# Kernel optimization log

Measured on AMD Instinct MI355X. Metric: run time of the kernel, lower is better.

The kernel has to match this reference:

```python
import jax, jax.numpy as jnp
import numpy as np

B, N, M, C = 2, 8192, 1024, 1152  # batch, dense points, centers, feature dim
K = 3                              # three_nn interpolation
EPS = 1e-8


def setup_inputs() -> dict:
    key = jax.random.key(0)
    k1, k2, k3 = jax.random.split(key, 3)
    xyz = jax.random.normal(k1, (B, N, 3), dtype=jnp.float32)      # query points
    center = jax.random.normal(k2, (B, M, 3), dtype=jnp.float32)   # center coords (already permuted to B,M,3)
    feats = jax.random.normal(k3, (B, C, M), dtype=jnp.float32)    # backbone features at centers
    return {"xyz": xyz, "center": center, "feats": feats}


def _interpolate(xyz, center, feats):
    # Squared pairwise distances [B, N, M] (PointNet++ three_nn uses squared dists).
    d2 = (jnp.sum(xyz * xyz, axis=-1, keepdims=True)
          + jnp.sum(center * center, axis=-1)[:, None, :]
          - 2.0 * jnp.einsum('bnd,bmd->bnm', xyz, center))
    neg_top, idx = jax.lax.top_k(-d2, K)          # 3 nearest centers per point
    dist = -neg_top                                # [B, N, K] squared distances
    recip = 1.0 / (dist + EPS)
    weight = recip / jnp.sum(recip, axis=-1, keepdims=True)  # [B, N, K]
    fm = jnp.transpose(feats, (0, 2, 1))           # [B, M, C]
    batch_idx = jnp.arange(B)[:, None, None]       # broadcast gather over batch
    gathered = fm[batch_idx, idx]                  # [B, N, K, C]
    out = jnp.einsum('bnkc,bnk->bcn', gathered, weight)  # [B, C, N]
    return out


def reference(xyz, center, feats):
    return _interpolate(xyz, center, feats)
```

## Files before the change

kernel.cpp:

```cpp
#include <hip/hip_runtime.h>
#include <cstdint>

#define B_ 2
#define N_ 8192
#define M_ 1024
#define C_ 1152
#define EPS_ 1e-8f
#define NT 32
#define CHUNK 128
#define NBN (N_ / NT)
#define NBC (C_ / CHUNK)
#define PTS 16
#define TRB ((M_ / 64) * (C_ / 64) * B_)

typedef float f32x4 __attribute__((ext_vector_type(4)));

__device__ __forceinline__ unsigned short f2bf(float f) {
    unsigned u = __float_as_uint(f);
    u += 0x7fffu + ((u >> 16) & 1u);
    return (unsigned short)(u >> 16);
}
__device__ __forceinline__ float bf2f(unsigned short h) {
    return __uint_as_float(((unsigned)h) << 16);
}

__device__ __forceinline__ void ins3(float d, int i,
        float& d0, int& i0, float& d1, int& i1, float& d2, int& i2) {
    bool b0 = d < d0;
    bool b1 = d < d1;
    bool b2 = d < d2;
    d2 = b1 ? d1 : (b2 ? d : d2);   i2 = b1 ? i1 : (b2 ? i : i2);
    d1 = b0 ? d0 : (b1 ? d : d1);   i1 = b0 ? i0 : (b1 ? i : i1);
    d0 = b0 ? d  : d0;              i0 = b0 ? i  : i0;
}
__device__ __forceinline__ void ins3lex(float d, int i,
        float& d0, int& i0, float& d1, int& i1, float& d2, int& i2) {
    bool b0 = (d < d0) || (d == d0 && i < i0);
    bool b1 = (d < d1) || (d == d1 && i < i1);
    bool b2 = (d < d2) || (d == d2 && i < i2);
    d2 = b1 ? d1 : (b2 ? d : d2);   i2 = b1 ? i1 : (b2 ? i : i2);
    d1 = b0 ? d0 : (b1 ? d : d1);   i1 = b0 ? i0 : (b1 ? i : i1);
    d0 = b0 ? d  : d0;              i0 = b0 ? i  : i0;
}

__global__ __launch_bounds__(256) void k_front(const float* __restrict__ feats,
                                               unsigned short* __restrict__ fm,
                                               const float* __restrict__ xyz,
                                               const float* __restrict__ center,
                                               int* __restrict__ idx_ws,
                                               float* __restrict__ w_ws) {
    __shared__ float4 sc[1040];
    int bid = blockIdx.x;
    int t   = threadIdx.x;

    if (bid < TRB) {
        float* tile = (float*)sc;
        int within = bid % ((M_ / 64) * (C_ / 64));
        int b  = bid / ((M_ / 64) * (C_ / 64));
        int mb = within & 15;
        int cb = within >> 4;
        int m0 = mb * 64;
        int c0 = cb * 64;
        int tx = t & 63;
        int ty = t >> 6;
        const float* src = feats + ((size_t)b * C_ + c0) * M_ + m0;
#pragma unroll
        for (int j = 0; j < 16; ++j) {
            int cl = ty + 4 * j;
            tile[cl * 65 + tx] = __builtin_nontemporal_load(&src[(size_t)cl * M_ + tx]);
        }
        __syncthreads();
        unsigned short* dst = fm + ((size_t)b * M_ + m0) * C_ + c0;
#pragma unroll
        for (int j = 0; j < 16; ++j) {
            int ml = ty + 4 * j;
            dst[(size_t)ml * C_ + tx] = f2bf(tile[tx * 65 + ml]);
        }
        return;
    }

    int flat = bid - TRB;
    int b    = flat >> 9;
    int n0   = (flat & 511) * PTS;
    for (int i = t; i < M_; i += 256) {
        float cx = center[((size_t)b * M_ + i) * 3 + 0];
        float cy = center[((size_t)b * M_ + i) * 3 + 1];
        float cz = center[((size_t)b * M_ + i) * 3 + 2];
        float cc = __fadd_rn(__fadd_rn(__fmul_rn(cx, cx), __fmul_rn(cy, cy)),
                             __fmul_rn(cz, cz));
        sc[i] = make_float4(cx, cy, cz, cc);
    }
    __syncthreads();

    int p = t >> 4;
    int c = t & 15;
    int n = n0 + p;
    float x = xyz[((size_t)b * N_ + n) * 3 + 0];
    float y = xyz[((size_t)b * N_ + n) * 3 + 1];
    float z = xyz[((size_t)b * N_ + n) * 3 + 2];
    float xx = __fadd_rn(__fadd_rn(__fmul_rn(x, x), __fmul_rn(y, y)),
                         __fmul_rn(z, z));

    float d0 = __builtin_inff(), d1 = __builtin_inff(), d2 = __builtin_inff();
    int   i0 = 0x7fffffff,  i1 = 0x7fffffff,  i2 = 0x7fffffff;
#pragma unroll 4
    for (int it = 0; it < M_ / 16; ++it) {
        int m = c + it * 16;
        float4 v = sc[m];
        float dot = __fmaf_rn(z, v.z, __fmaf_rn(y, v.y, __fmul_rn(x, v.x)));
        float d   = __fsub_rn(__fadd_rn(xx, v.w), __fmul_rn(2.0f, dot));
        ins3(d, m, d0, i0, d1, i1, d2, i2);
    }
#pragma unroll
    for (int off = 1; off <= 8; off <<= 1) {
        float e0 = __shfl_xor(d0, off); int j0 = __shfl_xor(i0, off);
        float e1 = __shfl_xor(d1, off); int j1 = __shfl_xor(i1, off);
        float e2 = __shfl_xor(d2, off); int j2 = __shfl_xor(i2, off);
        ins3lex(e0, j0, d0, i0, d1, i1, d2, i2);
        ins3lex(e1, j1, d0, i0, d1, i1, d2, i2);
        ins3lex(e2, j2, d0, i0, d1, i1, d2, i2);
    }
    if (c == 0) {
        float r0 = 1.0f / __fadd_rn(d0, EPS_);
        float r1 = 1.0f / __fadd_rn(d1, EPS_);
        float r2 = 1.0f / __fadd_rn(d2, EPS_);
        float s  = __fadd_rn(__fadd_rn(r0, r1), r2);
        size_t base = ((size_t)b * N_ + n) * 3;
        idx_ws[base + 0] = i0; idx_ws[base + 1] = i1; idx_ws[base + 2] = i2;
        w_ws[base + 0] = r0 / s; w_ws[base + 1] = r1 / s; w_ws[base + 2] = r2 / s;
    }
}

__global__ __launch_bounds__(256) void k_interp(const unsigned short* __restrict__ fm,
                                                const int* __restrict__ idx_ws,
                                                const float* __restrict__ w_ws,
                                                float* __restrict__ out) {
    __shared__ float T[NT][CHUNK + 1];
    __shared__ int   sbase[NT][3];
    __shared__ float sw[NT][3];
    int flat = blockIdx.x;
    int slot = flat & 7;
    int b    = slot >> 2;
    int idx  = (flat >> 3) * 4 + (slot & 3);
    int n0   = (idx & (NBN - 1)) * NT;
    int c0   = (idx >> 8) * CHUNK;
    int t    = threadIdx.x;
    if (t < NT) {
        size_t ib = ((size_t)b * N_ + n0 + t) * 3;
#pragma unroll
        for (int k = 0; k < 3; ++k) {
            sbase[t][k] = (b * M_ + idx_ws[ib + k]) * C_;
            sw[t][k]    = w_ws[ib + k];
        }
    }
    __syncthreads();
    int wave = t >> 6;
    int lane = t & 63;
    int half = lane >> 5;
    int cl   = (lane & 31) * 4;
#pragma unroll
    for (int pp = 0; pp < 4; ++pp) {
        int p = pp * 8 + wave * 2 + half;
        float w0 = sw[p][0], w1 = sw[p][1], w2 = sw[p][2];
        const ushort4 a0 = *(const ushort4*)(fm + sbase[p][0] + c0 + cl);
        const ushort4 a1 = *(const ushort4*)(fm + sbase[p][1] + c0 + cl);
        const ushort4 a2 = *(const ushort4*)(fm + sbase[p][2] + c0 + cl);
        T[p][cl + 0] = __fmaf_rn(bf2f(a2.x), w2, __fmaf_rn(bf2f(a1.x), w1, __fmul_rn(bf2f(a0.x), w0)));
        T[p][cl + 1] = __fmaf_rn(bf2f(a2.y), w2, __fmaf_rn(bf2f(a1.y), w1, __fmul_rn(bf2f(a0.y), w0)));
        T[p][cl + 2] = __fmaf_rn(bf2f(a2.z), w2, __fmaf_rn(bf2f(a1.z), w1, __fmul_rn(bf2f(a0.z), w0)));
        T[p][cl + 3] = __fmaf_rn(bf2f(a2.w), w2, __fmaf_rn(bf2f(a1.w), w1, __fmul_rn(bf2f(a0.w), w0)));
    }
    __syncthreads();
    int p4  = (t & 7) * 4;
    int ccb = t >> 3;
#pragma unroll
    for (int r = 0; r < 4; ++r) {
        int cc = r * 32 + ccb;
        f32x4 v = { T[p4 + 0][cc], T[p4 + 1][cc], T[p4 + 2][cc], T[p4 + 3][cc] };
        __builtin_nontemporal_store(v,
            (f32x4*)&out[((size_t)b * C_ + c0 + cc) * N_ + n0 + p4]);
    }
}

extern "C" void kernel_launch(void* const* d_in, const int* in_sizes, int n_in,
                              void* d_out, int out_size, void* d_ws, size_t ws_size,
                              hipStream_t stream) {
    const float* xyz    = (const float*)d_in[0];
    const float* center = (const float*)d_in[1];
    const float* feats  = (const float*)d_in[2];
    float* out = (float*)d_out;

    char*           ws     = (char*)d_ws;
    unsigned short* fm     = (unsigned short*)ws;
    int*            idx_ws = (int*)(ws + (size_t)B_ * M_ * C_ * 2);
    float*          w_ws   = (float*)(ws + (size_t)B_ * M_ * C_ * 2 + (size_t)B_ * N_ * 3 * 4);

    k_front <<<TRB + (N_ / PTS) * B_, 256, 0, stream>>>(feats, fm, xyz, center, idx_ws, w_ws);
    k_interp<<<NBN * NBC * B_, 256, 0, stream>>>(fm, idx_ws, w_ws, out);
}
```

Baseline: 37.32 us.

## Split three-NN into its own kernel with per-thread multi-point register blocking

The fused front kernel is split in two. A prep kernel transposes features to bf16 and packs the centers with their squared norms into a workspace buffer. A separate three-NN kernel has each thread handle 4 query points across 32 lanes, reading the packed centers straight from global/L2 with a software prefetch of the next center instead of staging them in shared memory. This reuses each center load across 4 points and cuts the shuffle-reduction work per point. The cost is an extra kernel launch, the loss of overlap between the transpose and the NN search, and more register pressure per thread.

Result: slower. 52.44 us (+40.5%).

```diff
diff --git a/kernel.cpp b/kernel.cpp
--- a/kernel.cpp
+++ b/kernel.cpp
@@ -10,8 +10,8 @@
 #define CHUNK 128
 #define NBN (N_ / NT)
 #define NBC (C_ / CHUNK)
-#define PTS 16
 #define TRB ((M_ / 64) * (C_ / 64) * B_)
+#define PTS 32
 
 typedef float f32x4 __attribute__((ext_vector_type(4)));
 
@@ -43,91 +43,131 @@
     d0 = b0 ? d  : d0;              i0 = b0 ? i  : i0;
 }
 
-__global__ __launch_bounds__(256) void k_front(const float* __restrict__ feats,
-                                               unsigned short* __restrict__ fm,
-                                               const float* __restrict__ xyz,
-                                               const float* __restrict__ center,
-                                               int* __restrict__ idx_ws,
-                                               float* __restrict__ w_ws) {
-    __shared__ float4 sc[1040];
+__global__ __launch_bounds__(256) void k_prep(const float* __restrict__ feats,
+                                              unsigned short* __restrict__ fm,
+                                              const float* __restrict__ center,
+                                              float4* __restrict__ cpk) {
+    __shared__ float tile[64][65];
     int bid = blockIdx.x;
     int t   = threadIdx.x;
 
-    if (bid < TRB) {
-        float* tile = (float*)sc;
-        int within = bid % ((M_ / 64) * (C_ / 64));
-        int b  = bid / ((M_ / 64) * (C_ / 64));
-        int mb = within & 15;
-        int cb = within >> 4;
-        int m0 = mb * 64;
-        int c0 = cb * 64;
-        int tx = t & 63;
-        int ty = t >> 6;
-        const float* src = feats + ((size_t)b * C_ + c0) * M_ + m0;
-#pragma unroll
-        for (int j = 0; j < 16; ++j) {
-            int cl = ty + 4 * j;
-            tile[cl * 65 + tx] = __builtin_nontemporal_load(&src[(size_t)cl * M_ + tx]);
-        }
-        __syncthreads();
-        unsigned short* dst = fm + ((size_t)b * M_ + m0) * C_ + c0;
-#pragma unroll
-        for (int j = 0; j < 16; ++j) {
-            int ml = ty + 4 * j;
-            dst[(size_t)ml * C_ + tx] = f2bf(tile[tx * 65 + ml]);
+    if (bid >= TRB) {
+        int b = bid - TRB;
+        for (int i = t; i < M_; i += 256) {
+            float cx = center[((size_t)b * M_ + i) * 3 + 0];
+            float cy = center[((size_t)b * M_ + i) * 3 + 1];
+            float cz = center[((size_t)b * M_ + i) * 3 + 2];
+            float cc = __fadd_rn(__fadd_rn(__fmul_rn(cx, cx), __fmul_rn(cy, cy)),
+                                 __fmul_rn(cz, cz));
+            cpk[b * M_ + i] = make_float4(cx, cy, cz, cc);
         }
         return;
     }
 
-    int flat = bid - TRB;
-    int b    = flat >> 9;
-    int n0   = (flat & 511) * PTS;
-    for (int i = t; i < M_; i += 256) {
-        float cx = center[((size_t)b * M_ + i) * 3 + 0];
-        float cy = center[((size_t)b * M_ + i) * 3 + 1];
-        float cz = center[((size_t)b * M_ + i) * 3 + 2];
-        float cc = __fadd_rn(__fadd_rn(__fmul_rn(cx, cx), __fmul_rn(cy, cy)),
-                             __fmul_rn(cz, cz));
-        sc[i] = make_float4(cx, cy, cz, cc);
+    int within = bid % ((M_ / 64) * (C_ / 64));
+    int b  = bid / ((M_ / 64) * (C_ / 64));
+    int mb = within & 15;
+    int cb = within >> 4;
+    int m0 = mb * 64;
+    int c0 = cb * 64;
+    int tx = t & 63;
+    int ty = t >> 6;
+    const float* src = feats + ((size_t)b * C_ + c0) * M_ + m0;
+#pragma unroll
+    for (int j = 0; j < 16; ++j) {
+        int cl = ty + 4 * j;
+        tile[cl][tx] = __builtin_nontemporal_load(&src[(size_t)cl * M_ + tx]);
     }
     __syncthreads();
-
-    int p = t >> 4;
-    int c = t & 15;
-    int n = n0 + p;
-    float x = xyz[((size_t)b * N_ + n) * 3 + 0];
-    float y = xyz[((size_t)b * N_ + n) * 3 + 1];
-    float z = xyz[((size_t)b * N_ + n) * 3 + 2];
-    float xx = __fadd_rn(__fadd_rn(__fmul_rn(x, x), __fmul_rn(y, y)),
-                         __fmul_rn(z, z));
-
-    float d0 = __builtin_inff(), d1 = __builtin_inff(), d2 = __builtin_inff();
-    int   i0 = 0x7fffffff,  i1 = 0x7fffffff,  i2 = 0x7fffffff;
-#pragma unroll 4
-    for (int it = 0; it < M_ / 16; ++it) {
-        int m = c + it * 16;
-        float4 v = sc[m];
-        float dot = __fmaf_rn(z, v.z, __fmaf_rn(y, v.y, __fmul_rn(x, v.x)));
-        float d   = __fsub_rn(__fadd_rn(xx, v.w), __fmul_rn(2.0f, dot));
-        ins3(d, m, d0, i0, d1, i1, d2, i2);
-    }
-#pragma unroll
-    for (int off = 1; off <= 8; off <<= 1) {
-        float e0 = __shfl_xor(d0, off); int j0 = __shfl_xor(i0, off);
-        float e1 = __shfl_xor(d1, off); int j1 = __shfl_xor(i1, off);
-        float e2 = __shfl_xor(d2, off); int j2 = __shfl_xor(i2, off);
-        ins3lex(e0, j0, d0, i0, d1, i1, d2, i2);
-        ins3lex(e1, j1, d0, i0, d1, i1, d2, i2);
-        ins3lex(e2, j2, d0, i0, d1, i1, d2, i2);
-    }
+    unsigned short* dst = fm + ((size_t)b * M_ + m0) * C_ + c0;
+#pragma unroll
+    for (int j = 0; j < 16; ++j) {
+        int ml = ty + 4 * j;
+        dst[(size_t)ml * C_ + tx] = f2bf(tile[tx][ml]);
+    }
+}
+
+__global__ __launch_bounds__(256) void k_threenn(const float* __restrict__ xyz,
+                                                 const float4* __restrict__ cpk,
+                                                 int* __restrict__ idx_ws,
+                                                 float* __restrict__ w_ws) {
+    int b  = blockIdx.y;
+    int n0 = blockIdx.x * PTS;
+    int t  = threadIdx.x;
+    int c  = t & 31;
+    int q  = t >> 5;
+    int n  = n0 + q * 4;
+
+    const float* xp = xyz + ((size_t)b * N_ + n) * 3;
+    f32x4 v0 = *(const f32x4*)(xp);
+    f32x4 v1 = *(const f32x4*)(xp + 4);
+    f32x4 v2 = *(const f32x4*)(xp + 8);
+    float px[4], py[4], pz[4], pxx[4];
+    px[0] = v0.x; py[0] = v0.y; pz[0] = v0.z;
+    px[1] = v0.w; py[1] = v1.x; pz[1] = v1.y;
+    px[2] = v1.z; py[2] = v1.w; pz[2] = v2.x;
+    px[3] = v2.y; py[3] = v2.z; pz[3] = v2.w;
+#pragma unroll
+    for (int k = 0; k < 4; ++k)
+        pxx[k] = __fadd_rn(__fadd_rn(__fmul_rn(px[k], px[k]), __fmul_rn(py[k], py[k])),
+                           __fmul_rn(pz[k], pz[k]));
+
+    float d0[4], d1[4], d2[4];
+    int   i0[4], i1[4], i2[4];
+#pragma unroll
+    for (int k = 0; k < 4; ++k) {
+        d0[k] = d1[k] = d2[k] = __builtin_inff();
+        i0[k] = i1[k] = i2[k] = 0x7fffffff;
+    }
+
+    const float4* cb = cpk + b * M_ + c;
+    float4 cur = cb[0];
+#pragma unroll 5
+    for (int it = 0; it < 31; ++it) {
+        float4 nxt = cb[(it + 1) * 32];
+        int m = c + it * 32;
+#pragma unroll
+        for (int k = 0; k < 4; ++k) {
+            float dot = __fmaf_rn(pz[k], cur.z, __fmaf_rn(py[k], cur.y, __fmul_rn(px[k], cur.x)));
+            float d   = __fsub_rn(__fadd_rn(pxx[k], cur.w), __fmul_rn(2.0f, dot));
+            ins3(d, m, d0[k], i0[k], d1[k], i1[k], d2[k], i2[k]);
+        }
+        cur = nxt;
+    }
+    {
+        int m = c + 31 * 32;
+#pragma unroll
+        for (int k = 0; k < 4; ++k) {
+            float dot = __fmaf_rn(pz[k], cur.z, __fmaf_rn(py[k], cur.y, __fmul_rn(px[k], cur.x)));
+            float d   = __fsub_rn(__fadd_rn(pxx[k], cur.w), __fmul_rn(2.0f, dot));
+            ins3(d, m, d0[k], i0[k], d1[k], i1[k], d2[k], i2[k]);
+        }
+    }
+
+#pragma unroll
+    for (int off = 1; off <= 16; off <<= 1) {
+#pragma unroll
+        for (int k = 0; k < 4; ++k) {
+            float e0 = __shfl_xor(d0[k], off); int j0 = __shfl_xor(i0[k], off);
+            float e1 = __shfl_xor(d1[k], off); int j1 = __shfl_xor(i1[k], off);
+            float e2 = __shfl_xor(d2[k], off); int j2 = __shfl_xor(i2[k], off);
+            ins3lex(e0, j0, d0[k], i0[k], d1[k], i1[k], d2[k], i2[k]);
+            ins3lex(e1, j1, d0[k], i0[k], d1[k], i1[k], d2[k], i2[k]);
+            ins3lex(e2, j2, d0[k], i0[k], d1[k], i1[k], d2[k], i2[k]);
+        }
+    }
+
     if (c == 0) {
-        float r0 = 1.0f / __fadd_rn(d0, EPS_);
-        float r1 = 1.0f / __fadd_rn(d1, EPS_);
-        float r2 = 1.0f / __fadd_rn(d2, EPS_);
-        float s  = __fadd_rn(__fadd_rn(r0, r1), r2);
-        size_t base = ((size_t)b * N_ + n) * 3;
-        idx_ws[base + 0] = i0; idx_ws[base + 1] = i1; idx_ws[base + 2] = i2;
-        w_ws[base + 0] = r0 / s; w_ws[base + 1] = r1 / s; w_ws[base + 2] = r2 / s;
+#pragma unroll
+        for (int k = 0; k < 4; ++k) {
+            float r0 = 1.0f / __fadd_rn(d0[k], EPS_);
+            float r1 = 1.0f / __fadd_rn(d1[k], EPS_);
+            float r2 = 1.0f / __fadd_rn(d2[k], EPS_);
+            float s  = __fadd_rn(__fadd_rn(r0, r1), r2);
+            size_t base = ((size_t)b * N_ + n + k) * 3;
+            idx_ws[base + 0] = i0[k]; idx_ws[base + 1] = i1[k]; idx_ws[base + 2] = i2[k];
+            w_ws[base + 0] = r0 / s; w_ws[base + 1] = r1 / s; w_ws[base + 2] = r2 / s;
+        }
     }
 }
 
@@ -192,9 +232,12 @@
 
     char*           ws     = (char*)d_ws;
     unsigned short* fm     = (unsigned short*)ws;
-    int*            idx_ws = (int*)(ws + (size_t)B_ * M_ * C_ * 2);
-    float*          w_ws   = (float*)(ws + (size_t)B_ * M_ * C_ * 2 + (size_t)B_ * N_ * 3 * 4);
-
-    k_front <<<TRB + (N_ / PTS) * B_, 256, 0, stream>>>(feats, fm, xyz, center, idx_ws, w_ws);
-    k_interp<<<NBN * NBC * B_, 256, 0, stream>>>(fm, idx_ws, w_ws, out);
-}
+    size_t off = (size_t)B_ * M_ * C_ * 2;
+    int*            idx_ws = (int*)(ws + off);      off += (size_t)B_ * N_ * 3 * 4;
+    float*          w_ws   = (float*)(ws + off);    off += (size_t)B_ * N_ * 3 * 4;
+    float4*         cpk    = (float4*)(ws + off);
+
+    k_prep   <<<TRB + B_, 256, 0, stream>>>(feats, fm, center, cpk);
+    k_threenn<<<dim3(N_ / PTS, B_), 256, 0, stream>>>(xyz, cpk, idx_ws, w_ws);
+    k_interp <<<NBN * NBC * B_, 256, 0, stream>>>(fm, idx_ws, w_ws, out);
+}
```

## Split front kernel into prep and three-NN kernels with precomputed center pack

Applied to the files above, without the earlier changes.

The fused front kernel is split in two. A prep kernel transposes the features to bf16 and packs each center with its squared norm into a float4 workspace. A separate three-NN kernel then loads that packed array into shared memory and handles 8 points per block with 32 lanes per point instead of 16, so twice as many blocks run. This removes the per-block recomputation of center norms and gives more parallelism in the search, at the cost of one extra kernel launch and a dependency that serializes the transpose before the search.

New measurement: 41.37 us. 10.9% more time.

```diff
diff --git a/kernel.cpp b/kernel.cpp
--- a/kernel.cpp
+++ b/kernel.cpp
@@ -10,8 +10,8 @@
 #define CHUNK 128
 #define NBN (N_ / NT)
 #define NBC (C_ / CHUNK)
-#define PTS 16
 #define TRB ((M_ / 64) * (C_ / 64) * B_)
+#define PTS 8
 
 typedef float f32x4 __attribute__((ext_vector_type(4)));
 
@@ -43,57 +43,66 @@
     d0 = b0 ? d  : d0;              i0 = b0 ? i  : i0;
 }
 
-__global__ __launch_bounds__(256) void k_front(const float* __restrict__ feats,
-                                               unsigned short* __restrict__ fm,
-                                               const float* __restrict__ xyz,
-                                               const float* __restrict__ center,
-                                               int* __restrict__ idx_ws,
-                                               float* __restrict__ w_ws) {
-    __shared__ float4 sc[1040];
+__global__ __launch_bounds__(256) void k_prep(const float* __restrict__ feats,
+                                              unsigned short* __restrict__ fm,
+                                              const float* __restrict__ center,
+                                              float4* __restrict__ cpk) {
+    __shared__ float tile[64][65];
     int bid = blockIdx.x;
     int t   = threadIdx.x;
 
-    if (bid < TRB) {
-        float* tile = (float*)sc;
-        int within = bid % ((M_ / 64) * (C_ / 64));
-        int b  = bid / ((M_ / 64) * (C_ / 64));
-        int mb = within & 15;
-        int cb = within >> 4;
-        int m0 = mb * 64;
-        int c0 = cb * 64;
-        int tx = t & 63;
-        int ty = t >> 6;
-        const float* src = feats + ((size_t)b * C_ + c0) * M_ + m0;
-#pragma unroll
-        for (int j = 0; j < 16; ++j) {
-            int cl = ty + 4 * j;
-            tile[cl * 65 + tx] = __builtin_nontemporal_load(&src[(size_t)cl * M_ + tx]);
-        }
-        __syncthreads();
-        unsigned short* dst = fm + ((size_t)b * M_ + m0) * C_ + c0;
-#pragma unroll
-        for (int j = 0; j < 16; ++j) {
-            int ml = ty + 4 * j;
-            dst[(size_t)ml * C_ + tx] = f2bf(tile[tx * 65 + ml]);
+    if (bid >= TRB) {
+        int b = bid - TRB;
+        for (int i = t; i < M_; i += 256) {
+            float cx = center[((size_t)b * M_ + i) * 3 + 0];
+            float cy = center[((size_t)b * M_ + i) * 3 + 1];
+            float cz = center[((size_t)b * M_ + i) * 3 + 2];
+            float cc = __fadd_rn(__fadd_rn(__fmul_rn(cx, cx), __fmul_rn(cy, cy)),
+                                 __fmul_rn(cz, cz));
+            cpk[b * M_ + i] = make_float4(cx, cy, cz, cc);
         }
         return;
     }
 
-    int flat = bid - TRB;
-    int b    = flat >> 9;
-    int n0   = (flat & 511) * PTS;
-    for (int i = t; i < M_; i += 256) {
-        float cx = center[((size_t)b * M_ + i) * 3 + 0];
-        float cy = center[((size_t)b * M_ + i) * 3 + 1];
-        float cz = center[((size_t)b * M_ + i) * 3 + 2];
-        float cc = __fadd_rn(__fadd_rn(__fmul_rn(cx, cx), __fmul_rn(cy, cy)),
-                             __fmul_rn(cz, cz));
-        sc[i] = make_float4(cx, cy, cz, cc);
-    }
-    __syncthreads();
-
-    int p = t >> 4;
-    int c = t & 15;
+    int within = bid % ((M_ / 64) * (C_ / 64));
+    int b  = bid / ((M_ / 64) * (C_ / 64));
+    int mb = within & 15;
+    int cb = within >> 4;
+    int m0 = mb * 64;
+    int c0 = cb * 64;
+    int tx = t & 63;
+    int ty = t >> 6;
+    const float* src = feats + ((size_t)b * C_ + c0) * M_ + m0;
+#pragma unroll
+    for (int j = 0; j < 16; ++j) {
+        int cl = ty + 4 * j;
+        tile[cl][tx] = __builtin_nontemporal_load(&src[(size_t)cl * M_ + tx]);
+    }
+    __syncthreads();
+    unsigned short* dst = fm + ((size_t)b * M_ + m0) * C_ + c0;
+#pragma unroll
+    for (int j = 0; j < 16; ++j) {
+        int ml = ty + 4 * j;
+        dst[(size_t)ml * C_ + tx] = f2bf(tile[tx][ml]);
+    }
+}
+
+__global__ __launch_bounds__(256) void k_threenn(const float* __restrict__ xyz,
+                                                 const float4* __restrict__ cpk,
+                                                 int* __restrict__ idx_ws,
+                                                 float* __restrict__ w_ws) {
+    __shared__ float4 sc[M_];
+    int b  = blockIdx.y;
+    int n0 = blockIdx.x * PTS;
+    int t  = threadIdx.x;
+    const float4* src = cpk + (size_t)b * M_;
+#pragma unroll
+    for (int i = 0; i < 4; ++i)
+        sc[t + i * 256] = src[t + i * 256];
+    __syncthreads();
+
+    int p = t >> 5;
+    int c = t & 31;
     int n = n0 + p;
     float x = xyz[((size_t)b * N_ + n) * 3 + 0];
     float y = xyz[((size_t)b * N_ + n) * 3 + 1];
@@ -104,15 +113,15 @@
     float d0 = __builtin_inff(), d1 = __builtin_inff(), d2 = __builtin_inff();
     int   i0 = 0x7fffffff,  i1 = 0x7fffffff,  i2 = 0x7fffffff;
 #pragma unroll 4
-    for (int it = 0; it < M_ / 16; ++it) {
-        int m = c + it * 16;
+    for (int it = 0; it < M_ / 32; ++it) {
+        int m = c + it * 32;
         float4 v = sc[m];
         float dot = __fmaf_rn(z, v.z, __fmaf_rn(y, v.y, __fmul_rn(x, v.x)));
         float d   = __fsub_rn(__fadd_rn(xx, v.w), __fmul_rn(2.0f, dot));
         ins3(d, m, d0, i0, d1, i1, d2, i2);
     }
 #pragma unroll
-    for (int off = 1; off <= 8; off <<= 1) {
+    for (int off = 1; off <= 16; off <<= 1) {
         float e0 = __shfl_xor(d0, off); int j0 = __shfl_xor(i0, off);
         float e1 = __shfl_xor(d1, off); int j1 = __shfl_xor(i1, off);
         float e2 = __shfl_xor(d2, off); int j2 = __shfl_xor(i2, off);
@@ -192,9 +201,12 @@
 
     char*           ws     = (char*)d_ws;
     unsigned short* fm     = (unsigned short*)ws;
-    int*            idx_ws = (int*)(ws + (size_t)B_ * M_ * C_ * 2);
-    float*          w_ws   = (float*)(ws + (size_t)B_ * M_ * C_ * 2 + (size_t)B_ * N_ * 3 * 4);
-
-    k_front <<<TRB + (N_ / PTS) * B_, 256, 0, stream>>>(feats, fm, xyz, center, idx_ws, w_ws);
-    k_interp<<<NBN * NBC * B_, 256, 0, stream>>>(fm, idx_ws, w_ws, out);
-}
+    size_t off = (size_t)B_ * M_ * C_ * 2;
+    int*            idx_ws = (int*)(ws + off);      off += (size_t)B_ * N_ * 3 * 4;
+    float*          w_ws   = (float*)(ws + off);    off += (size_t)B_ * N_ * 3 * 4;
+    float4*         cpk    = (float4*)(ws + off);
+
+    k_prep   <<<TRB + B_, 256, 0, stream>>>(feats, fm, center, cpk);
+    k_threenn<<<dim3(N_ / PTS, B_), 256, 0, stream>>>(xyz, cpk, idx_ws, w_ws);
+    k_interp <<<NBN * NBC * B_, 256, 0, stream>>>(fm, idx_ws, w_ws, out);
+}
```

## Restructure nearest-neighbor search: per-lane points, wave-split centers, prepacked center buffer

Applied to the files above, without the earlier changes.

Adds a small kernel that packs the centers into float4 records with precomputed squared norms. The kNN part of k_front now gives one query point to each lane and splits the centers across 8 waves, reading them as wave-uniform scalar loads from global memory instead of staging them in LDS. Each wave's top-3 candidates are merged through shared memory, and the sorted insert uses fmin/med3. Blocks grow to 512 threads and kNN blocks are scheduled ahead of the transpose blocks. This removes the per-block center staging and the shuffle reduction, but adds a kernel launch and an LDS merge step, and leaves only 256 kNN blocks.

Measured after the change: 43.51 us. 16.6% more time.

```diff
diff --git a/kernel.cpp b/kernel.cpp
--- a/kernel.cpp
+++ b/kernel.cpp
@@ -10,8 +10,9 @@
 #define CHUNK 128
 #define NBN (N_ / NT)
 #define NBC (C_ / CHUNK)
-#define PTS 16
 #define TRB ((M_ / 64) * (C_ / 64) * B_)
+#define NNB 256
+#define CW  (M_ / 8)
 
 typedef float f32x4 __attribute__((ext_vector_type(4)));
 
@@ -24,15 +25,6 @@
     return __uint_as_float(((unsigned)h) << 16);
 }
 
-__device__ __forceinline__ void ins3(float d, int i,
-        float& d0, int& i0, float& d1, int& i1, float& d2, int& i2) {
-    bool b0 = d < d0;
-    bool b1 = d < d1;
-    bool b2 = d < d2;
-    d2 = b1 ? d1 : (b2 ? d : d2);   i2 = b1 ? i1 : (b2 ? i : i2);
-    d1 = b0 ? d0 : (b1 ? d : d1);   i1 = b0 ? i0 : (b1 ? i : i1);
-    d0 = b0 ? d  : d0;              i0 = b0 ? i  : i0;
-}
 __device__ __forceinline__ void ins3lex(float d, int i,
         float& d0, int& i0, float& d1, int& i1, float& d2, int& i2) {
     bool b0 = (d < d0) || (d == d0 && i < i0);
@@ -43,20 +35,32 @@
     d0 = b0 ? d  : d0;              i0 = b0 ? i  : i0;
 }
 
-__global__ __launch_bounds__(256) void k_front(const float* __restrict__ feats,
+__global__ __launch_bounds__(256) void k_pack(const float* __restrict__ center,
+                                              float4* __restrict__ cpk) {
+    int i = blockIdx.x * 256 + threadIdx.x;
+    float cx = center[(size_t)i * 3 + 0];
+    float cy = center[(size_t)i * 3 + 1];
+    float cz = center[(size_t)i * 3 + 2];
+    float cc = __fadd_rn(__fadd_rn(__fmul_rn(cx, cx), __fmul_rn(cy, cy)),
+                         __fmul_rn(cz, cz));
+    cpk[i] = make_float4(cx, cy, cz, cc);
+}
+
+__global__ __launch_bounds__(512) void k_front(const float* __restrict__ feats,
                                                unsigned short* __restrict__ fm,
                                                const float* __restrict__ xyz,
-                                               const float* __restrict__ center,
+                                               const float4* __restrict__ cpk,
                                                int* __restrict__ idx_ws,
                                                float* __restrict__ w_ws) {
-    __shared__ float4 sc[1040];
+    __shared__ float4 shb[1040];
     int bid = blockIdx.x;
     int t   = threadIdx.x;
 
-    if (bid < TRB) {
-        float* tile = (float*)sc;
-        int within = bid % ((M_ / 64) * (C_ / 64));
-        int b  = bid / ((M_ / 64) * (C_ / 64));
+    if (bid >= NNB) {
+        float* tile = (float*)shb;
+        int tb = bid - NNB;
+        int within = tb % ((M_ / 64) * (C_ / 64));
+        int b  = tb / ((M_ / 64) * (C_ / 64));
         int mb = within & 15;
         int cb = within >> 4;
         int m0 = mb * 64;
@@ -65,68 +69,81 @@
         int ty = t >> 6;
         const float* src = feats + ((size_t)b * C_ + c0) * M_ + m0;
 #pragma unroll
-        for (int j = 0; j < 16; ++j) {
-            int cl = ty + 4 * j;
+        for (int j = 0; j < 8; ++j) {
+            int cl = ty + 8 * j;
             tile[cl * 65 + tx] = __builtin_nontemporal_load(&src[(size_t)cl * M_ + tx]);
         }
         __syncthreads();
         unsigned short* dst = fm + ((size_t)b * M_ + m0) * C_ + c0;
 #pragma unroll
-        for (int j = 0; j < 16; ++j) {
-            int ml = ty + 4 * j;
+        for (int j = 0; j < 8; ++j) {
+            int ml = ty + 8 * j;
             dst[(size_t)ml * C_ + tx] = f2bf(tile[tx * 65 + ml]);
         }
         return;
     }
 
-    int flat = bid - TRB;
-    int b    = flat >> 9;
-    int n0   = (flat & 511) * PTS;
-    for (int i = t; i < M_; i += 256) {
-        float cx = center[((size_t)b * M_ + i) * 3 + 0];
-        float cy = center[((size_t)b * M_ + i) * 3 + 1];
-        float cz = center[((size_t)b * M_ + i) * 3 + 2];
-        float cc = __fadd_rn(__fadd_rn(__fmul_rn(cx, cx), __fmul_rn(cy, cy)),
-                             __fmul_rn(cz, cz));
-        sc[i] = make_float4(cx, cy, cz, cc);
-    }
-    __syncthreads();
-
-    int p = t >> 4;
-    int c = t & 15;
-    int n = n0 + p;
-    float x = xyz[((size_t)b * N_ + n) * 3 + 0];
-    float y = xyz[((size_t)b * N_ + n) * 3 + 1];
-    float z = xyz[((size_t)b * N_ + n) * 3 + 2];
+    int b  = bid >> 7;
+    int n0 = (bid & 127) * 64;
+    int w  = t >> 6;
+    int l  = t & 63;
+    int n  = n0 + l;
+
+    const float* xp = xyz + ((size_t)b * N_ + n) * 3;
+    float x = xp[0], y = xp[1], z = xp[2];
     float xx = __fadd_rn(__fadd_rn(__fmul_rn(x, x), __fmul_rn(y, y)),
                          __fmul_rn(z, z));
 
+    int cbase = __builtin_amdgcn_readfirstlane(b * M_ + w * CW);
+    int mbase = __builtin_amdgcn_readfirstlane(w * CW);
+
     float d0 = __builtin_inff(), d1 = __builtin_inff(), d2 = __builtin_inff();
     int   i0 = 0x7fffffff,  i1 = 0x7fffffff,  i2 = 0x7fffffff;
-#pragma unroll 4
-    for (int it = 0; it < M_ / 16; ++it) {
-        int m = c + it * 16;
-        float4 v = sc[m];
+#pragma unroll 8
+    for (int it = 0; it < CW; ++it) {
+        float4 v = cpk[cbase + it];
+        int m = mbase + it;
         float dot = __fmaf_rn(z, v.z, __fmaf_rn(y, v.y, __fmul_rn(x, v.x)));
-        float d   = __fsub_rn(__fadd_rn(xx, v.w), __fmul_rn(2.0f, dot));
-        ins3(d, m, d0, i0, d1, i1, d2, i2);
-    }
-#pragma unroll
-    for (int off = 1; off <= 8; off <<= 1) {
-        float e0 = __shfl_xor(d0, off); int j0 = __shfl_xor(i0, off);
-        float e1 = __shfl_xor(d1, off); int j1 = __shfl_xor(i1, off);
-        float e2 = __shfl_xor(d2, off); int j2 = __shfl_xor(i2, off);
-        ins3lex(e0, j0, d0, i0, d1, i1, d2, i2);
-        ins3lex(e1, j1, d0, i0, d1, i1, d2, i2);
-        ins3lex(e2, j2, d0, i0, d1, i1, d2, i2);
-    }
-    if (c == 0) {
-        float r0 = 1.0f / __fadd_rn(d0, EPS_);
-        float r1 = 1.0f / __fadd_rn(d1, EPS_);
-        float r2 = 1.0f / __fadd_rn(d2, EPS_);
+        float s0  = __fadd_rn(xx, v.w);
+        float d   = __fmaf_rn(-2.0f, dot, s0);
+        bool b0 = d < d0;
+        bool b1 = d < d1;
+        bool b2 = d < d2;
+        float nd0 = fminf(d, d0);
+        float nd1 = __builtin_amdgcn_fmed3f(d, d0, d1);
+        float nd2 = __builtin_amdgcn_fmed3f(d, d1, d2);
+        i2 = b1 ? i1 : (b2 ? m : i2);
+        i1 = b0 ? i0 : (b1 ? m : i1);
+        i0 = b0 ? m  : i0;
+        d0 = nd0; d1 = nd1; d2 = nd2;
+    }
+
+    float* cand = (float*)shb;
+    int cb2 = (w * 64 + l) * 6;
+    cand[cb2 + 0] = d0; ((int*)cand)[cb2 + 1] = i0;
+    cand[cb2 + 2] = d1; ((int*)cand)[cb2 + 3] = i1;
+    cand[cb2 + 4] = d2; ((int*)cand)[cb2 + 5] = i2;
+    __syncthreads();
+
+    if (w == 0) {
+        float D0 = __builtin_inff(), D1 = __builtin_inff(), D2 = __builtin_inff();
+        int   I0 = 0x7fffffff,  I1 = 0x7fffffff,  I2 = 0x7fffffff;
+#pragma unroll
+        for (int ww = 0; ww < 8; ++ww) {
+            int rb = (ww * 64 + l) * 6;
+            float e0 = cand[rb + 0]; int j0 = ((int*)cand)[rb + 1];
+            float e1 = cand[rb + 2]; int j1 = ((int*)cand)[rb + 3];
+            float e2 = cand[rb + 4]; int j2 = ((int*)cand)[rb + 5];
+            ins3lex(e0, j0, D0, I0, D1, I1, D2, I2);
+            ins3lex(e1, j1, D0, I0, D1, I1, D2, I2);
+            ins3lex(e2, j2, D0, I0, D1, I1, D2, I2);
+        }
+        float r0 = 1.0f / __fadd_rn(D0, EPS_);
+        float r1 = 1.0f / __fadd_rn(D1, EPS_);
+        float r2 = 1.0f / __fadd_rn(D2, EPS_);
         float s  = __fadd_rn(__fadd_rn(r0, r1), r2);
         size_t base = ((size_t)b * N_ + n) * 3;
-        idx_ws[base + 0] = i0; idx_ws[base + 1] = i1; idx_ws[base + 2] = i2;
+        idx_ws[base + 0] = I0; idx_ws[base + 1] = I1; idx_ws[base + 2] = I2;
         w_ws[base + 0] = r0 / s; w_ws[base + 1] = r1 / s; w_ws[base + 2] = r2 / s;
     }
 }
@@ -192,9 +209,12 @@
 
     char*           ws     = (char*)d_ws;
     unsigned short* fm     = (unsigned short*)ws;
-    int*            idx_ws = (int*)(ws + (size_t)B_ * M_ * C_ * 2);
-    float*          w_ws   = (float*)(ws + (size_t)B_ * M_ * C_ * 2 + (size_t)B_ * N_ * 3 * 4);
-
-    k_front <<<TRB + (N_ / PTS) * B_, 256, 0, stream>>>(feats, fm, xyz, center, idx_ws, w_ws);
+    size_t off = (size_t)B_ * M_ * C_ * 2;
+    int*            idx_ws = (int*)(ws + off);      off += (size_t)B_ * N_ * 3 * 4;
+    float*          w_ws   = (float*)(ws + off);    off += (size_t)B_ * N_ * 3 * 4;
+    float4*         cpk    = (float4*)(ws + off);
+
+    k_pack  <<<(B_ * M_) / 256, 256, 0, stream>>>(center, cpk);
+    k_front <<<NNB + TRB, 512, 0, stream>>>(feats, fm, xyz, cpk, idx_ws, w_ws);
     k_interp<<<NBN * NBC * B_, 256, 0, stream>>>(fm, idx_ws, w_ws, out);
 }
```
